# Performance work log

Hardware: AMD Instinct MI355X
Metric: run time of the kernel (lower is better)

## Reference

```python
import jax, jax.numpy as jnp
import numpy as np

D_MODEL = 2048
H = 16
D_K = D_MODEL // H


def setup_inputs() -> dict:
    key = jax.random.key(0)
    ks = jax.random.split(key, 9)
    b, n, d = 2, 2048, D_MODEL
    s = 1.0 / np.sqrt(d)
    return {
        "x": jax.random.normal(ks[0], (b, n, d), jnp.float32),
        "Wq": jax.random.normal(ks[1], (d, d), jnp.float32) * s,
        "bq": jax.random.normal(ks[2], (d,), jnp.float32) * 0.01,
        "Wk": jax.random.normal(ks[3], (d, d), jnp.float32) * s,
        "bk": jax.random.normal(ks[4], (d,), jnp.float32) * 0.01,
        "Wv": jax.random.normal(ks[5], (d, d), jnp.float32) * s,
        "bv": jax.random.normal(ks[6], (d,), jnp.float32) * 0.01,
        "Wo": jax.random.normal(ks[7], (d, d), jnp.float32) * s,
        "bo": jax.random.normal(ks[8], (d,), jnp.float32) * 0.01,
    }


def reference(x, Wq, bq, Wk, bk, Wv, bv, Wo, bo):
    b, n, d = x.shape
    h, dk = H, D_K

    def split_heads(t):
        return t.reshape(b, n, h, dk).transpose(0, 2, 1, 3)  # (b,h,n,dk)

    q = split_heads(x @ Wq + bq)
    k = split_heads(x @ Wk + bk)
    v = split_heads(x @ Wv + bv)

    scores = jnp.einsum("bhqd,bhkd->bhqk", q, k) / jnp.sqrt(jnp.float32(dk))
    causal = jnp.tril(jnp.ones((n, n), dtype=bool))  # (n,n)
    scores = jnp.where(causal[None, None], scores, -jnp.inf)
    attn = jax.nn.softmax(scores, axis=-1)  # dropout = identity (eval)

    out = jnp.einsum("bhqk,bhkd->bhqd", attn, v)
    out = out.transpose(0, 2, 1, 3).reshape(b, n, d)
    return out @ Wo + bo
```

## Files before the change

kernel.cpp:

```cpp
#include <hip/hip_runtime.h>

typedef unsigned short u16;
typedef unsigned int u32;
typedef __attribute__((ext_vector_type(8))) short short8;
typedef __attribute__((ext_vector_type(4))) float f32x4;
typedef __attribute__((ext_vector_type(16))) float f32x16;
typedef __attribute__((ext_vector_type(4))) u16 u16x4;
typedef __attribute__((ext_vector_type(4))) u32 u32x4;

#define QK_SCALE 0.12751736915185197f

__device__ __forceinline__ u16 f2bf(float f) {
  u32 u = __builtin_bit_cast(u32, f);
  u = u + 0x7FFFu + ((u >> 16) & 1u);
  return (u16)(u >> 16);
}

__device__ __forceinline__ void async_copy16(const void* g, void* l) {
  __builtin_amdgcn_global_load_lds(
      (const __attribute__((address_space(1))) u32*)g,
      (__attribute__((address_space(3))) u32*)l, 16, 0, 0);
}

#define VMCNT(n) asm volatile("s_waitcnt vmcnt(" #n ")" ::: "memory")

__global__ __launch_bounds__(256) void cast_x_kernel(const float* __restrict__ x,
                                                     u16* __restrict__ xb, int n) {
  int i = (blockIdx.x * 256 + threadIdx.x) * 8;
  if (i >= n) return;
  float4 a = *(const float4*)(x + i);
  float4 b = *(const float4*)(x + i + 4);
  short8 o;
  o[0] = (short)f2bf(a.x); o[1] = (short)f2bf(a.y);
  o[2] = (short)f2bf(a.z); o[3] = (short)f2bf(a.w);
  o[4] = (short)f2bf(b.x); o[5] = (short)f2bf(b.y);
  o[6] = (short)f2bf(b.z); o[7] = (short)f2bf(b.w);
  *(short8*)(xb + i) = o;
}

__global__ __launch_bounds__(256) void transW_kernel(
    const float* __restrict__ W0, const float* __restrict__ W1,
    const float* __restrict__ W2, const float* __restrict__ W3,
    u16* __restrict__ O0, u16* __restrict__ O1, u16* __restrict__ O2, u16* __restrict__ O3) {
  const float* Ws[4] = {W0, W1, W2, W3};
  u16* Os[4] = {O0, O1, O2, O3};
  const float* W = Ws[blockIdx.z];
  u16* O = Os[blockIdx.z];

  __shared__ float T[64][65];
  int t = threadIdx.x;
  int k0 = blockIdx.y * 64, n0 = blockIdx.x * 64;
  int r = t >> 4, c = (t & 15) * 4;
#pragma unroll
  for (int i = 0; i < 4; ++i) {
    float4 v = *(const float4*)&W[(size_t)(k0 + r + i * 16) * 2048 + n0 + c];
    T[r + i * 16][c + 0] = v.x; T[r + i * 16][c + 1] = v.y;
    T[r + i * 16][c + 2] = v.z; T[r + i * 16][c + 3] = v.w;
  }
  __syncthreads();
#pragma unroll
  for (int i = 0; i < 4; ++i) {
    int nn = r + i * 16;
    u16x4 o;
    o[0] = f2bf(T[c + 0][nn]); o[1] = f2bf(T[c + 1][nn]);
    o[2] = f2bf(T[c + 2][nn]); o[3] = f2bf(T[c + 3][nn]);
    *(u16x4*)&O[(size_t)(n0 + nn) * 2048 + k0 + c] = o;
  }
}

__global__ __launch_bounds__(256) void transV_kernel(const u16* __restrict__ V,
                                                     u16* __restrict__ Vt) {
  int bh = blockIdx.y;
  int n0 = blockIdx.x * 64;
  const u16* Vb = V + (size_t)bh * 262144;
  u16* Ob = Vt + (size_t)bh * 262144;
  __shared__ u16 T[64 * 129];
  int t = threadIdx.x;
#pragma unroll
  for (int j = 0; j < 4; ++j) {
    int p = t + j * 256;
    int r = p >> 4, c = (p & 15) * 8;
    short8 v = *(const short8*)(Vb + (size_t)(n0 + r) * 128 + c);
#pragma unroll
    for (int e = 0; e < 8; ++e) T[r * 129 + c + e] = (u16)v[e];
  }
  __syncthreads();
#pragma unroll
  for (int pass = 0; pass < 4; ++pass) {
    int dk = (t >> 3) + pass * 32;
    int cn = (t & 7) * 8;
    short8 o;
#pragma unroll
    for (int e = 0; e < 8; ++e) o[e] = (short)T[(cn + e) * 129 + dk];
    *(short8*)(Ob + (size_t)dk * 2048 + n0 + cn) = o;
  }
}

template <int MODE>
__global__ __launch_bounds__(512, 2) void gemm8p_kernel(
    const u16* __restrict__ A, const u16* __restrict__ W,
    const float* __restrict__ b0, const float* __restrict__ b1, const float* __restrict__ b2,
    u16* __restrict__ oq, u16* __restrict__ ok, u16* __restrict__ ov,
    float* __restrict__ of) {
  __shared__ __align__(16) u16 SM[73728];

  int t = threadIdx.x;
  int lane = t & 63, w = t >> 6;
  int wm = w >> 2, wn = w & 3;
  int g = lane >> 4, lr = lane & 15;
  int m0 = blockIdx.y * 128, n0 = blockIdx.x * 256;

  int sArow = ((t >> 8) << 6) + ((t >> 3) & 31);
  int c8A = (t & 7) ^ ((t >> 3) & 7);
  const u16* Asrc = A + (size_t)(m0 + sArow) * 2048 + c8A * 8;
  int rB = t >> 3;
  int c8B = (t & 7) ^ (rB & 7);
  const u16* Bsrc = W + (size_t)(n0 + rB) * 2048 + c8B * 8;

  int ko0 = (g ^ (lr & 7)) * 8;
  int ko1 = ((4 + g) ^ (lr & 7)) * 8;
  int offA[4], offB[4];
#pragma unroll
  for (int mf = 0; mf < 4; ++mf)
    offA[mf] = (mf >> 1) * 4096 + wm * 2048 + ((mf & 1) * 16 + lr) * 64;
#pragma unroll
  for (int nf = 0; nf < 4; ++nf)
    offB[nf] = 8192 + (wn >> 1) * 8192 + ((wn & 1) * 64 + nf * 16 + lr) * 64;

  f32x4 acc[4][4] = {};

#define STG_A(sbuf, mh, kt) \
  async_copy16(Asrc + (mh) * 65536 + (kt), (void*)(SM + (sbuf) + (mh) * 4096 + t * 8))
#define STG_B(sbuf, half, kt)                                                          \
  do {                                                                                 \
    async_copy16(Bsrc + (half) * 262144 + (kt),                                        \
                 (void*)(SM + (sbuf) + 8192 + (half) * 8192 + t * 8));                 \
    async_copy16(Bsrc + (half) * 262144 + 131072 + (kt),                               \
                 (void*)(SM + (sbuf) + 8192 + (half) * 8192 + 4096 + t * 8));          \
  } while (0)

  STG_A(0, 0, 0); STG_B(0, 0, 0);
  STG_A(0, 1, 0); STG_B(0, 1, 0);
  STG_A(24576, 0, 64); STG_B(24576, 0, 64);
  STG_A(24576, 1, 64); STG_B(24576, 1, 64);
  VMCNT(6);
  __builtin_amdgcn_s_barrier();

  u32 cb = 0, sb = 49152;
  for (int tt = 0; tt < 32; ++tt) {
    int kt2 = (tt + 2) << 6;
    bool stg = tt < 30;
    const u16* Bu = SM + cb;

    short8 af[2][2], bfr[4][2];
#pragma unroll
    for (int m2 = 0; m2 < 2; ++m2) {
      af[m2][0] = *(const short8*)&Bu[offA[m2] + ko0];
      af[m2][1] = *(const short8*)&Bu[offA[m2] + ko1];
    }
#pragma unroll
    for (int nf = 0; nf < 4; ++nf) {
      bfr[nf][0] = *(const short8*)&Bu[offB[nf] + ko0];
      bfr[nf][1] = *(const short8*)&Bu[offB[nf] + ko1];
    }
    if (stg) { STG_A(sb, 0, kt2); STG_B(sb, 0, kt2); }
    __builtin_amdgcn_s_barrier();
    asm volatile("s_waitcnt lgkmcnt(0)" ::: "memory");
    __builtin_amdgcn_sched_barrier(0);
    __builtin_amdgcn_s_setprio(1);
#pragma unroll
    for (int kk = 0; kk < 2; ++kk)
#pragma unroll
      for (int m2 = 0; m2 < 2; ++m2)
#pragma unroll
        for (int nf = 0; nf < 4; ++nf)
          acc[m2][nf] =
              __builtin_amdgcn_mfma_f32_16x16x32_bf16(af[m2][kk], bfr[nf][kk], acc[m2][nf], 0, 0, 0);
    __builtin_amdgcn_s_setprio(0);
    __builtin_amdgcn_s_barrier();

#pragma unroll
    for (int m2 = 0; m2 < 2; ++m2) {
      af[m2][0] = *(const short8*)&Bu[offA[2 + m2] + ko0];
      af[m2][1] = *(const short8*)&Bu[offA[2 + m2] + ko1];
    }
    if (stg) { STG_A(sb, 1, kt2); STG_B(sb, 1, kt2); }
    __builtin_amdgcn_s_barrier();
    asm volatile("s_waitcnt lgkmcnt(0)" ::: "memory");
    __builtin_amdgcn_sched_barrier(0);
    __builtin_amdgcn_s_setprio(1);
#pragma unroll
    for (int kk = 0; kk < 2; ++kk)
#pragma unroll
      for (int m2 = 0; m2 < 2; ++m2)
#pragma unroll
        for (int nf = 0; nf < 4; ++nf)
          acc[2 + m2][nf] = __builtin_amdgcn_mfma_f32_16x16x32_bf16(af[m2][kk], bfr[nf][kk],
                                                                    acc[2 + m2][nf], 0, 0, 0);
    __builtin_amdgcn_s_setprio(0);
    if (tt < 30) { VMCNT(6); } else { VMCNT(0); }
    __builtin_amdgcn_s_barrier();

    cb += 24576; if (cb == 73728) cb = 0;
    sb += 24576; if (sb == 73728) sb = 0;
  }
#undef STG_A
#undef STG_B

  int zsel = n0 >> 11;
  const float* bias = (zsel == 0) ? b0 : (zsel == 1) ? b1 : b2;
  u16* outb = (MODE == 0) ? ((zsel == 0) ? oq : (zsel == 1) ? ok : ov) : nullptr;
#pragma unroll
  for (int mf = 0; mf < 4; ++mf) {
#pragma unroll
    for (int nf = 0; nf < 4; ++nf) {
      int col = n0 + wn * 64 + nf * 16 + lr;
      int cc = col & 2047;
      float bv = bias[cc];
#pragma unroll
      for (int i = 0; i < 4; ++i) {
        int rr = m0 + wm * 64 + mf * 16 + 4 * g + i;
        float v = acc[mf][nf][i] + bv;
        if (MODE == 0) {
          int b = rr >> 11, np = rr & 2047, h = cc >> 7, dk = cc & 127;
          outb[((size_t)(b * 16 + h) * 2048 + np) * 128 + dk] = f2bf(v);
        } else {
          of[(size_t)rr * 2048 + col] = v;
        }
      }
    }
  }
}

__global__ __launch_bounds__(256, 2) void attn_kernel(
    const u16* __restrict__ Q, const u16* __restrict__ K, const u16* __restrict__ Vt,
    u16* __restrict__ ctx) {
  int bh = blockIdx.y;
  int q0 = (int)(gridDim.x - 1 - blockIdx.x) * 128;
  int t = threadIdx.x, lane = t & 63, w = t >> 6;
  int h = lane >> 5;
  int ql = lane & 31;
  int q0w = q0 + w * 32;
  int qg = q0w + ql;

  const u16* Qb = Q + (size_t)bh * 262144;
  const u16* Kb = K + (size_t)bh * 262144;
  const u16* Vb = Vt + (size_t)bh * 262144;

  __shared__ __align__(16) u16 SM[32768];

  short8 qf[8];
  {
    const u16* qrow = Qb + (size_t)qg * 128 + 8 * h;
#pragma unroll
    for (int kk = 0; kk < 8; ++kk) qf[kk] = *(const short8*)(qrow + 16 * kk);
  }

  f32x16 acc[4] = {};
  float m = -1e30f, lsum = 0.f;

  int nt = (q0 + 128) >> 6;
  int wave_max = q0w + 31;

  auto STAGE = [&](int buf, int kv0) {
    u16* Ksb = SM + buf * 16384;
    u16* Vsb = Ksb + 8192;
#pragma unroll
    for (int it = 0; it < 4; ++it) {
      int p = t + 256 * it;
      int row = p >> 4;
      int c = (p & 15) ^ (row & 15);
      async_copy16(Kb + (size_t)(kv0 + row) * 128 + c * 8, (void*)(Ksb + p * 8));
      async_copy16(Vb + (size_t)(2 * row + (c >> 3)) * 2048 + kv0 + (c & 7) * 8,
                   (void*)(Vsb + p * 8));
    }
  };

  STAGE(0, 0);
  __syncthreads();

  for (int step = 0; step < nt; ++step) {
    int kv0 = step << 6;
    int cur = step & 1;
    if (step + 1 < nt) STAGE(cur ^ 1, (step + 1) << 6);

    if (kv0 <= wave_max) {
      const u16* Ksb = SM + cur * 16384;
      const u16* Vsb = Ksb + 8192;

      f32x16 s0 = {}, s1 = {};
#pragma unroll
      for (int kk = 0; kk < 8; ++kk) {
        int c = (2 * kk + h) ^ (ql & 15);
        short8 kf0 = *(const short8*)&Ksb[ql * 128 + c * 8];
        s0 = __builtin_amdgcn_mfma_f32_32x32x16_bf16(kf0, qf[kk], s0, 0, 0, 0);
        short8 kf1 = *(const short8*)&Ksb[(32 + ql) * 128 + c * 8];
        s1 = __builtin_amdgcn_mfma_f32_32x32x16_bf16(kf1, qf[kk], s1, 0, 0, 0);
      }

      if (kv0 + 63 > q0w) {
#pragma unroll
        for (int r = 0; r < 16; ++r) {
          int slot = (r & 3) + 8 * (r >> 2) + 4 * h;
          if (kv0 + slot > qg) s0[r] = -1e30f;
          if (kv0 + 32 + slot > qg) s1[r] = -1e30f;
        }
      }

      float tm = fmaxf(s0[0], s1[0]);
#pragma unroll
      for (int r = 1; r < 16; ++r) tm = fmaxf(tm, fmaxf(s0[r], s1[r]));
      tm = fmaxf(tm, __shfl_xor(tm, 32));
      tm *= QK_SCALE;

      if (__any(tm > m + 8.0f)) {
        float mn = fmaxf(m, tm);
        float rr = exp2f(m - mn);
        m = mn;
        lsum *= rr;
#pragma unroll
        for (int d = 0; d < 4; ++d)
#pragma unroll
          for (int i = 0; i < 16; ++i) acc[d][i] *= rr;
      }

      float rs = 0.f;
#pragma unroll
      for (int r = 0; r < 16; ++r) {
        s0[r] = exp2f(fmaf(s0[r], QK_SCALE, -m));
        s1[r] = exp2f(fmaf(s1[r], QK_SCALE, -m));
        rs += s0[r] + s1[r];
      }
      rs += __shfl_xor(rs, 32);
      lsum += rs;

      u32 up0[8], up1[8];
#pragma unroll
      for (int mi = 0; mi < 8; ++mi) {
        asm("v_cvt_pk_bf16_f32 %0, %1, %2" : "=v"(up0[mi]) : "v"(s0[2 * mi]), "v"(s0[2 * mi + 1]));
        asm("v_cvt_pk_bf16_f32 %0, %1, %2" : "=v"(up1[mi]) : "v"(s1[2 * mi]), "v"(s1[2 * mi + 1]));
      }

#pragma unroll
      for (int g16 = 0; g16 < 4; ++g16) {
        int Qd = g16 & 1;
        u32 c0 = (g16 < 2) ? up0[4 * Qd + 0] : up1[4 * Qd + 0];
        u32 c1 = (g16 < 2) ? up0[4 * Qd + 1] : up1[4 * Qd + 1];
        u32 c2 = (g16 < 2) ? up0[4 * Qd + 2] : up1[4 * Qd + 2];
        u32 c3 = (g16 < 2) ? up0[4 * Qd + 3] : up1[4 * Qd + 3];
        u32 d0 = __shfl_xor(c0, 32), d1 = __shfl_xor(c1, 32);
        u32 d2 = __shfl_xor(c2, 32), d3 = __shfl_xor(c3, 32);
        u32x4 paw;
        paw[0] = h ? d2 : c0;
        paw[1] = h ? d3 : c1;
        paw[2] = h ? c2 : d0;
        paw[3] = h ? c3 : d1;
        short8 pa = __builtin_bit_cast(short8, paw);
#pragma unroll
        for (int d = 0; d < 4; ++d) {
          int dk = 32 * d + ql;
          int prow = dk >> 1;
          int lch = (dk & 1) * 8 + 2 * g16 + h;
          int slot = lch ^ (prow & 15);
          short8 vf = *(const short8*)&Vsb[prow * 128 + slot * 8];
          acc[d] = __builtin_amdgcn_mfma_f32_32x32x16_bf16(vf, pa, acc[d], 0, 0, 0);
        }
      }
    }
    __syncthreads();
  }

  u16* Ot = SM + w * 4352;
  float inv = 1.f / lsum;
#pragma unroll
  for (int d = 0; d < 4; ++d)
#pragma unroll
    for (int r = 0; r < 16; ++r) {
      int dk = 32 * d + (r & 3) + 8 * (r >> 2) + 4 * h;
      Ot[ql * 136 + dk] = f2bf(acc[d][r] * inv);
    }
  __syncthreads();
  int b = bh >> 4, hh = bh & 15;
#pragma unroll
  for (int it = 0; it < 8; ++it) {
    int p = lane + 64 * it;
    int row = p >> 4, ch = p & 15;
    short8 v = *(const short8*)&Ot[row * 136 + ch * 8];
    *(short8*)(ctx + ((size_t)(b * 2048 + q0 + w * 32 + row)) * 2048 + hh * 128 + ch * 8) = v;
  }
}

extern "C" void kernel_launch(void* const* d_in, const int* in_sizes, int n_in,
                              void* d_out, int out_size, void* d_ws, size_t ws_size,
                              hipStream_t stream) {
  const float* x = (const float*)d_in[0];
  const float* Wq = (const float*)d_in[1];
  const float* bq = (const float*)d_in[2];
  const float* Wk = (const float*)d_in[3];
  const float* bk = (const float*)d_in[4];
  const float* Wv = (const float*)d_in[5];
  const float* bv = (const float*)d_in[6];
  const float* Wo = (const float*)d_in[7];
  const float* bo = (const float*)d_in[8];
  float* out = (float*)d_out;

  u16* xb = (u16*)d_ws;
  u16* WTq = xb + 8388608;
  u16* WTk = WTq + 4194304;
  u16* WTv = WTk + 4194304;
  u16* WTo = WTv + 4194304;
  u16* Qs = WTo + 4194304;
  u16* Ks = Qs + 8388608;
  u16* Vs = Ks + 8388608;
  u16* ctx = Vs + 8388608;
  u16* Vt = xb;

  cast_x_kernel<<<4096, 256, 0, stream>>>(x, xb, 8388608);
  transW_kernel<<<dim3(32, 32, 4), 256, 0, stream>>>(Wq, Wk, Wv, Wo, WTq, WTk, WTv, WTo);
  gemm8p_kernel<0><<<dim3(24, 32), 512, 0, stream>>>(
      xb, WTq, bq, bk, bv, Qs, Ks, Vs, nullptr);
  transV_kernel<<<dim3(32, 32), 256, 0, stream>>>(Vs, Vt);
  attn_kernel<<<dim3(16, 32), 256, 0, stream>>>(Qs, Ks, Vt, ctx);
  gemm8p_kernel<1><<<dim3(8, 32), 512, 0, stream>>>(
      ctx, WTo, bo, bo, bo, nullptr, nullptr, nullptr, out);
}
```

Before: 267.6 us.

## Use 256x256 tiles with an 8-phase double-buffered pipeline for the QKV GEMM

Adds a dedicated QKV projection kernel that computes 256x256 output tiles per block instead of 128x256, with 8 waves each owning 128x64. It double-buffers 64-wide K slices in 128 KB of LDS and spreads the staging of the next tiles across 8 MFMA phases. The larger tile raises arithmetic intensity and halves the B-operand reloads. In exchange the grid shrinks to 384 blocks, each wave holds more accumulator registers, and there is one block per CU. The output projection moves into its own non-templated kernel that keeps the old schedule.

New measurement: 266.3 us. Within noise of the previous version (-0.5%).

```diff
diff --git a/kernel.cpp b/kernel.cpp
--- a/kernel.cpp
+++ b/kernel.cpp
@@ -96,12 +96,117 @@
   }
 }
 
-template <int MODE>
-__global__ __launch_bounds__(512, 2) void gemm8p_kernel(
+__global__ __launch_bounds__(512, 2) void gemm256_kernel(
     const u16* __restrict__ A, const u16* __restrict__ W,
     const float* __restrict__ b0, const float* __restrict__ b1, const float* __restrict__ b2,
-    u16* __restrict__ oq, u16* __restrict__ ok, u16* __restrict__ ov,
-    float* __restrict__ of) {
+    u16* __restrict__ oq, u16* __restrict__ ok, u16* __restrict__ ov) {
+  __shared__ __align__(16) u16 SM[65536];
+
+  int t = threadIdx.x;
+  int lane = t & 63, w = t >> 6;
+  int wm = w >> 2, wn = w & 3;
+  int g = lane >> 4, lr = lane & 15;
+  int m0 = blockIdx.y * 256, n0 = blockIdx.x * 256;
+
+  const u16* AsrcB = A + (size_t)(m0 + (t >> 3)) * 2048 + ((t & 7) ^ ((t >> 3) & 7)) * 8;
+  const u16* BsrcB = W + (size_t)(n0 + (t >> 3)) * 2048 + ((t & 7) ^ ((t >> 3) & 7)) * 8;
+  int t8 = t * 8;
+
+  int ko0 = (g ^ (lr & 7)) * 8;
+  int ko1 = ((4 + g) ^ (lr & 7)) * 8;
+  int aoff[8], boff[4];
+#pragma unroll
+  for (int mf = 0; mf < 8; ++mf) aoff[mf] = (wm * 128 + mf * 16 + lr) * 64;
+#pragma unroll
+  for (int nf = 0; nf < 4; ++nf) boff[nf] = (wn * 64 + nf * 16 + lr) * 64;
+
+  f32x4 acc[8][4] = {};
+  short8 af[2][2], bfr[4][2];
+
+#define SA(b, j, tl) \
+  async_copy16(AsrcB + (size_t)(j) * 131072 + (tl) * 64, (void*)(SM + (b) * 32768 + (j) * 4096 + t8))
+#define SB(b, j, tl) \
+  async_copy16(BsrcB + (size_t)(j) * 131072 + (tl) * 64, \
+               (void*)(SM + (b) * 32768 + 16384 + (j) * 4096 + t8))
+
+#define PHASE(hbuf, q, STAGE_OPS, VM_OP)                                        \
+  {                                                                             \
+    const u16* Ab = SM + (hbuf) * 32768;                                        \
+    const u16* Bb = Ab + 16384;                                                 \
+    af[0][0] = *(const short8*)&Ab[aoff[2 * (q)] + ko0];                        \
+    af[0][1] = *(const short8*)&Ab[aoff[2 * (q)] + ko1];                        \
+    af[1][0] = *(const short8*)&Ab[aoff[2 * (q) + 1] + ko0];                    \
+    af[1][1] = *(const short8*)&Ab[aoff[2 * (q) + 1] + ko1];                    \
+    if ((q) == 0) {                                                             \
+      _Pragma("unroll") for (int nf = 0; nf < 4; ++nf) {                        \
+        bfr[nf][0] = *(const short8*)&Bb[boff[nf] + ko0];                       \
+        bfr[nf][1] = *(const short8*)&Bb[boff[nf] + ko1];                       \
+      }                                                                         \
+    }                                                                           \
+    STAGE_OPS;                                                                  \
+    __builtin_amdgcn_s_barrier();                                               \
+    asm volatile("s_waitcnt lgkmcnt(0)" ::: "memory");                          \
+    __builtin_amdgcn_sched_barrier(0);                                          \
+    __builtin_amdgcn_s_setprio(1);                                              \
+    _Pragma("unroll") for (int kk = 0; kk < 2; ++kk)                            \
+        _Pragma("unroll") for (int m2 = 0; m2 < 2; ++m2)                        \
+            _Pragma("unroll") for (int nf = 0; nf < 4; ++nf)                    \
+                acc[2 * (q) + m2][nf] = __builtin_amdgcn_mfma_f32_16x16x32_bf16(\
+                    af[m2][kk], bfr[nf][kk], acc[2 * (q) + m2][nf], 0, 0, 0);   \
+    __builtin_amdgcn_s_setprio(0);                                              \
+    VM_OP;                                                                      \
+    __builtin_amdgcn_s_barrier();                                               \
+  }
+
+  SB(0, 0, 0); SB(0, 1, 0); SB(0, 2, 0); SB(0, 3, 0);
+  SA(0, 0, 0); SA(0, 2, 0); SA(0, 1, 0); SA(0, 3, 0);
+  SB(1, 0, 1); SB(1, 1, 1); SB(1, 2, 1); SB(1, 3, 1);
+  SA(1, 0, 1); SA(1, 2, 1);
+  VMCNT(6);
+  __builtin_amdgcn_s_barrier();
+
+  for (int i = 0; i < 16; ++i) {
+    bool more = i < 15;
+    int t1 = 2 * i + 1, t2 = 2 * i + 2, t3 = 2 * i + 3;
+    PHASE(0, 0, { SA(1, 1, t1); SA(1, 3, t1); }, {});
+    PHASE(0, 1, { if (more) { SB(0, 0, t2); SB(0, 1, t2); } }, {});
+    PHASE(0, 2, { if (more) { SB(0, 2, t2); SB(0, 3, t2); } }, {});
+    PHASE(0, 3, { if (more) { SA(0, 0, t2); SA(0, 2, t2); } },
+          { if (more) { VMCNT(6); } else { VMCNT(0); } });
+    PHASE(1, 0, { if (more) { SA(0, 1, t2); SA(0, 3, t2); } }, {});
+    PHASE(1, 1, { if (more) { SB(1, 0, t3); SB(1, 1, t3); } }, {});
+    PHASE(1, 2, { if (more) { SB(1, 2, t3); SB(1, 3, t3); } }, {});
+    PHASE(1, 3, { if (more) { SA(1, 0, t3); SA(1, 2, t3); } },
+          { if (more) { VMCNT(6); } else { VMCNT(0); } });
+  }
+#undef PHASE
+#undef SA
+#undef SB
+
+  int zsel = n0 >> 11;
+  const float* bias = (zsel == 0) ? b0 : (zsel == 1) ? b1 : b2;
+  u16* outb = (zsel == 0) ? oq : (zsel == 1) ? ok : ov;
+#pragma unroll
+  for (int mf = 0; mf < 8; ++mf) {
+#pragma unroll
+    for (int nf = 0; nf < 4; ++nf) {
+      int col = n0 + wn * 64 + nf * 16 + lr;
+      int cc = col & 2047;
+      float bv = bias[cc];
+#pragma unroll
+      for (int i = 0; i < 4; ++i) {
+        int rr = m0 + wm * 128 + mf * 16 + 4 * g + i;
+        float v = acc[mf][nf][i] + bv;
+        int b = rr >> 11, np = rr & 2047, h = cc >> 7, dk = cc & 127;
+        outb[((size_t)(b * 16 + h) * 2048 + np) * 128 + dk] = f2bf(v);
+      }
+    }
+  }
+}
+
+__global__ __launch_bounds__(512, 2) void gemmO_kernel(
+    const u16* __restrict__ A, const u16* __restrict__ W,
+    const float* __restrict__ bias, float* __restrict__ of) {
   __shared__ __align__(16) u16 SM[73728];
 
   int t = threadIdx.x;
@@ -131,12 +236,12 @@
 
 #define STG_A(sbuf, mh, kt) \
   async_copy16(Asrc + (mh) * 65536 + (kt), (void*)(SM + (sbuf) + (mh) * 4096 + t * 8))
-#define STG_B(sbuf, half, kt)                                                          \
-  do {                                                                                 \
-    async_copy16(Bsrc + (half) * 262144 + (kt),                                        \
-                 (void*)(SM + (sbuf) + 8192 + (half) * 8192 + t * 8));                 \
-    async_copy16(Bsrc + (half) * 262144 + 131072 + (kt),                               \
-                 (void*)(SM + (sbuf) + 8192 + (half) * 8192 + 4096 + t * 8));          \
+#define STG_B(sbuf, half, kt)                                                 \
+  do {                                                                        \
+    async_copy16(Bsrc + (half) * 262144 + (kt),                               \
+                 (void*)(SM + (sbuf) + 8192 + (half) * 8192 + t * 8));        \
+    async_copy16(Bsrc + (half) * 262144 + 131072 + (kt),                      \
+                 (void*)(SM + (sbuf) + 8192 + (half) * 8192 + 4096 + t * 8)); \
   } while (0)
 
   STG_A(0, 0, 0); STG_B(0, 0, 0);
@@ -207,26 +312,16 @@
 #undef STG_A
 #undef STG_B
 
-  int zsel = n0 >> 11;
-  const float* bias = (zsel == 0) ? b0 : (zsel == 1) ? b1 : b2;
-  u16* outb = (MODE == 0) ? ((zsel == 0) ? oq : (zsel == 1) ? ok : ov) : nullptr;
 #pragma unroll
   for (int mf = 0; mf < 4; ++mf) {
 #pragma unroll
     for (int nf = 0; nf < 4; ++nf) {
       int col = n0 + wn * 64 + nf * 16 + lr;
-      int cc = col & 2047;
-      float bv = bias[cc];
+      float bv = bias[col];
 #pragma unroll
       for (int i = 0; i < 4; ++i) {
         int rr = m0 + wm * 64 + mf * 16 + 4 * g + i;
-        float v = acc[mf][nf][i] + bv;
-        if (MODE == 0) {
-          int b = rr >> 11, np = rr & 2047, h = cc >> 7, dk = cc & 127;
-          outb[((size_t)(b * 16 + h) * 2048 + np) * 128 + dk] = f2bf(v);
-        } else {
-          of[(size_t)rr * 2048 + col] = v;
-        }
+        of[(size_t)rr * 2048 + col] = acc[mf][nf][i] + bv;
       }
     }
   }
@@ -417,10 +512,8 @@
 
   cast_x_kernel<<<4096, 256, 0, stream>>>(x, xb, 8388608);
   transW_kernel<<<dim3(32, 32, 4), 256, 0, stream>>>(Wq, Wk, Wv, Wo, WTq, WTk, WTv, WTo);
-  gemm8p_kernel<0><<<dim3(24, 32), 512, 0, stream>>>(
-      xb, WTq, bq, bk, bv, Qs, Ks, Vs, nullptr);
+  gemm256_kernel<<<dim3(24, 16), 512, 0, stream>>>(xb, WTq, bq, bk, bv, Qs, Ks, Vs);
   transV_kernel<<<dim3(32, 32), 256, 0, stream>>>(Vs, Vt);
   attn_kernel<<<dim3(16, 32), 256, 0, stream>>>(Qs, Ks, Vt, ctx);
-  gemm8p_kernel<1><<<dim3(8, 32), 512, 0, stream>>>(
-      ctx, WTo, bo, bo, bo, nullptr, nullptr, nullptr, out);
-}
+  gemmO_kernel<<<dim3(8, 32), 512, 0, stream>>>(ctx, WTo, bo, out);
+}
```
